# Kernel tuning notes

Hardware: AMD Instinct MI355X
Metric: run time of the kernel (lower is better)

The kernel has to match this reference:

```python
import jax, jax.numpy as jnp
import numpy as np

N_HEADS = 4
N_HIDDEN = 128  # out_features, is_concat=False
NEG_SLOPE = 0.2


def setup_inputs() -> dict:
    key = jax.random.key(0)
    k1, k2, k3, k4 = jax.random.split(key, 4)
    A, S, P, F = 128, 64, 16, 128
    h = jax.random.normal(k1, (A, S, P, F), dtype=jnp.float32)
    # torch Linear(in, out, bias=False): y = x @ W.T ; here we store W already transposed [in, out]
    scale = 1.0 / np.sqrt(F)
    W_l = jax.random.normal(k2, (F, N_HEADS * N_HIDDEN), dtype=jnp.float32) * scale
    W_r = jax.random.normal(k3, (F, N_HEADS * N_HIDDEN), dtype=jnp.float32) * scale
    w_attn = jax.random.normal(k4, (2 * N_HIDDEN,), dtype=jnp.float32) * (1.0 / np.sqrt(2 * N_HIDDEN))
    return {"h": h, "W_l": W_l, "W_r": W_r, "w_attn": w_attn}


def reference(h, W_l, W_r, w_attn):
    A, S, P, F = h.shape
    H, D = N_HEADS, N_HIDDEN
    h_ = jnp.transpose(h, (1, 2, 0, 3))  # [S,P,A,F]
    g_l = (h_ @ W_l).reshape(S, P, A, H, D)
    g_r = (h_ @ W_r).reshape(S, P, A, H, D)
    # attn(cat(g_l[j], g_r[i])) = <w_attn[:D], g_l[j]> + <w_attn[D:], g_r[i]>
    # (single-output Linear over concat, shared across heads) — identical math,
    # avoids materializing the [S,P,A,A,H,2D] concat tensor.
    a_l, a_r = w_attn[:D], w_attn[D:]
    s_l = jnp.einsum('spahd,d->spah', g_l, a_l)  # contributes along j axis
    s_r = jnp.einsum('spahd,d->spah', g_r, a_r)  # contributes along i axis
    e = s_r[:, :, :, None, :] + s_l[:, :, None, :, :]  # [S,P,i,j,H]
    e = jax.nn.leaky_relu(e, negative_slope=NEG_SLOPE)
    diag = jnp.eye(A, dtype=bool)[None, None, :, :, None]  # mask self-edges
    e = jnp.where(diag, -jnp.inf, e)
    a = jax.nn.softmax(e, axis=3)  # softmax over j
    attn_res = jnp.einsum('spijh,spjhd->spihd', a, g_r)  # [S,P,A,H,D]
    attn_res = attn_res.mean(axis=3)  # is_concat=False -> mean over heads
    attn_res = jnp.transpose(attn_res, (2, 0, 1, 3))  # [A,S,P,D]
    return attn_res, a
```

## Files before the change

### kernel.cpp

```cpp
#include <hip/hip_runtime.h>
#include <hip/hip_bf16.h>
#include <stdint.h>


typedef short short8 __attribute__((ext_vector_type(8)));
typedef float f32x4 __attribute__((ext_vector_type(4)));

__device__ __forceinline__ float bf2f(unsigned short u) {
    return __uint_as_float(((unsigned int)u) << 16);
}
__device__ __forceinline__ unsigned short f2bf(float f) {
    unsigned int x = __float_as_uint(f);
    return (unsigned short)((x + 0x7FFFu + ((x >> 16) & 1u)) >> 16);
}
__device__ __forceinline__ float lrelu(float x) {
    return fmaxf(x, 0.2f * x);
}

__global__ void gat_precomp(const float* __restrict__ Wl,
                            const float* __restrict__ Wr,
                            const float* __restrict__ wattn,
                            unsigned short* __restrict__ Wt,
                            float* __restrict__ Vl,
                            float* __restrict__ Vr) {
    int b = blockIdx.x, t = threadIdx.x;
    if (b < 64) {
        int base = b * 1024 + t * 4;
        float4 v = *(const float4*)(Wr + base);
        int f = base >> 9;
        int c = base & 511;
        Wt[(c + 0) * 128 + f] = f2bf(v.x);
        Wt[(c + 1) * 128 + f] = f2bf(v.y);
        Wt[(c + 2) * 128 + f] = f2bf(v.z);
        Wt[(c + 3) * 128 + f] = f2bf(v.w);
    } else {
        const float* W  = (b == 64) ? Wl : Wr;
        const float* aw = wattn + ((b == 64) ? 0 : 128);
        float* V = (b == 64) ? Vl : Vr;
        for (int r = 0; r < 2; ++r) {
            int o = t + r * 256;
            int f = o >> 2, hh = o & 3;
            float acc = 0.f;
            for (int d = 0; d < 128; ++d)
                acc += W[f * 512 + hh * 128 + d] * aw[d];
            V[hh * 128 + f] = acc;
        }
    }
}

__global__ __launch_bounds__(512, 6)
void gat_main(const float* __restrict__ hin,
              const unsigned short* __restrict__ Wt,
              const float* __restrict__ Vl,
              const float* __restrict__ Vr,
              float* __restrict__ out_attn,
              float* __restrict__ out_a) {
    __shared__ __align__(16) unsigned short Gs[128][136];
    __shared__ float sLs[4][132];
    __shared__ float sRs[4][132];
    __shared__ float Ms[4][132];
    __shared__ float Siv[4][132];
    __shared__ float mx1[4], mx2[4];
    __shared__ int   ax1[4];

    const int sp = blockIdx.x;
    const int t = threadIdx.x;
    const int w = t >> 6;
    const int l = t & 63;
    const int q = l >> 4;
    const int ln = l & 15;

    {
        int a = t >> 2, hh = t & 3;
        const float* hr = hin + (size_t)a * 131072 + sp * 128;
        const float* vl = Vl + hh * 128;
        const float* vr = Vr + hh * 128;
        float al = 0.f, ar = 0.f;
        for (int f = 0; f < 128; f += 4) {
            float4 x  = *(const float4*)(hr + f);
            float4 a4 = *(const float4*)(vl + f);
            float4 b4 = *(const float4*)(vr + f);
            al += x.x * a4.x + x.y * a4.y + x.z * a4.z + x.w * a4.w;
            ar += x.x * b4.x + x.y * b4.y + x.z * b4.z + x.w * b4.w;
        }
        sLs[hh][a] = al;
        sRs[hh][a] = ar;
    }
    __syncthreads();

    if (w < 4) {
        float v0 = sLs[w][l], v1 = sLs[w][l + 64];
        float m1, m2; int a1;
        if (v0 >= v1) { m1 = v0; m2 = v1; a1 = l; }
        else          { m1 = v1; m2 = v0; a1 = l + 64; }
        #pragma unroll
        for (int off = 32; off; off >>= 1) {
            float o1 = __shfl_down(m1, off);
            float o2 = __shfl_down(m2, off);
            int   ob = __shfl_down(a1, off);
            if (o1 > m1) { m2 = fmaxf(m1, o2); m1 = o1; a1 = ob; }
            else         { m2 = fmaxf(m2, o1); }
        }
        if (l == 0) { mx1[w] = m1; mx2[w] = m2; ax1[w] = a1; }
    }
    __syncthreads();

    {
        int i = t >> 2, hh = t & 3;
        float sr = sRs[hh][i];
        float Mi = (i == ax1[hh]) ? mx2[hh] : mx1[hh];
        float m = lrelu(sr + Mi);
        float sum = 0.f;
        for (int j = 0; j < 128; ++j) {
            float e = lrelu(sr + sLs[hh][j]);
            sum += __expf(e - m);
        }
        sum -= __expf(lrelu(sr + sLs[hh][i]) - m);
        Ms[hh][i] = m;
        Siv[hh][i] = 1.f / sum;
    }
    __syncthreads();

    {
        float* oa = out_a + (size_t)sp * 65536;
        for (int k = 0; k < 32; ++k) {
            int idx = k * 512 + t;
            int i = idx >> 7, j = idx & 127;
            float4 r4;
            float* rp = (float*)&r4;
            #pragma unroll
            for (int hh = 0; hh < 4; ++hh) {
                float pv = 0.f;
                if (j != i) {
                    float e = lrelu(sRs[hh][i] + sLs[hh][j]);
                    pv = __expf(e - Ms[hh][i]) * Siv[hh][i];
                }
                rp[hh] = pv;
            }
            *(float4*)(oa + (size_t)idx * 4) = r4;
        }
    }

    f32x4 acc[8];
    #pragma unroll
    for (int tj = 0; tj < 8; ++tj) acc[tj] = (f32x4){0.f, 0.f, 0.f, 0.f};

    const float* hrw = hin + (size_t)(16 * w + ln) * 131072 + sp * 128;

    for (int hh = 0; hh < 4; ++hh) {
        __syncthreads();

        short8 axh[4];
        #pragma unroll
        for (int kb = 0; kb < 4; ++kb) {
            float4 xa = *(const float4*)(hrw + 32 * kb + 8 * q);
            float4 xb = *(const float4*)(hrw + 32 * kb + 8 * q + 4);
            short8 v;
            v[0] = (short)f2bf(xa.x); v[1] = (short)f2bf(xa.y);
            v[2] = (short)f2bf(xa.z); v[3] = (short)f2bf(xa.w);
            v[4] = (short)f2bf(xb.x); v[5] = (short)f2bf(xb.y);
            v[6] = (short)f2bf(xb.z); v[7] = (short)f2bf(xb.w);
            axh[kb] = v;
        }

        #pragma unroll
        for (int tj = 0; tj < 8; ++tj) {
            f32x4 g = (f32x4){0.f, 0.f, 0.f, 0.f};
            #pragma unroll
            for (int kb = 0; kb < 4; ++kb) {
                short8 bh = *(const short8*)(Wt + ((hh * 128 + 16 * tj + ln) * 128 + 32 * kb + 8 * q));
                g = __builtin_amdgcn_mfma_f32_16x16x32_bf16(axh[kb], bh, g, 0, 0, 0);
            }
            ushort4 gh4;
            unsigned short* ghp = (unsigned short*)&gh4;
            #pragma unroll
            for (int r = 0; r < 4; ++r) ghp[r] = f2bf(g[r]);
            *(ushort4*)(&Gs[16 * tj + ln][16 * w + 4 * q]) = gh4;
        }
        __syncthreads();

        {
            const int i = 16 * w + ln;
            const float sr = sRs[hh][i];
            const float m = Ms[hh][i];
            const float si = Siv[hh][i];
            #pragma unroll 1
            for (int kb = 0; kb < 4; ++kb) {
                short8 ph, pl;
                #pragma unroll
                for (int jj = 0; jj < 8; ++jj) {
                    int j = 32 * kb + 8 * q + jj;
                    float pv = 0.f;
                    if (j != i) {
                        float e = lrelu(sr + sLs[hh][j]);
                        pv = __expf(e - m) * si;
                    }
                    unsigned short hb = f2bf(pv);
                    ph[jj] = (short)hb;
                    pl[jj] = (short)f2bf(pv - bf2f(hb));
                }
                #pragma unroll
                for (int tj = 0; tj < 8; ++tj) {
                    short8 bh = *(const short8*)(&Gs[16 * tj + ln][32 * kb + 8 * q]);
                    acc[tj] = __builtin_amdgcn_mfma_f32_16x16x32_bf16(ph, bh, acc[tj], 0, 0, 0);
                    acc[tj] = __builtin_amdgcn_mfma_f32_16x16x32_bf16(pl, bh, acc[tj], 0, 0, 0);
                }
            }
        }
    }

    #pragma unroll
    for (int tj = 0; tj < 8; ++tj) {
        int d = 16 * tj + ln;
        #pragma unroll
        for (int r = 0; r < 4; ++r) {
            int i = 16 * w + 4 * q + r;
            out_attn[((size_t)i * 1024 + sp) * 128 + d] = acc[tj][r] * 0.25f;
        }
    }
}

extern "C" void kernel_launch(void* const* d_in, const int* in_sizes, int n_in,
                              void* d_out, int out_size, void* d_ws, size_t ws_size,
                              hipStream_t stream) {
    const float* hin   = (const float*)d_in[0];
    const float* Wl    = (const float*)d_in[1];
    const float* Wr    = (const float*)d_in[2];
    const float* wattn = (const float*)d_in[3];

    unsigned short* Wt = (unsigned short*)d_ws;
    float* Vl = (float*)((char*)d_ws + 131072);
    float* Vr = (float*)((char*)d_ws + 131072 + 2048);

    float* out_attn = (float*)d_out;
    float* out_a    = (float*)d_out + 16777216;

    gat_precomp<<<66, 256, 0, stream>>>(Wl, Wr, wattn, Wt, Vl, Vr);
    gat_main<<<1024, 512, 0, stream>>>(hin, Wt, Vl, Vr, out_attn, out_a);
}
```

Before: 550.1 us.

## Split output feature dimension into halves to cut LDS and registers, raise occupancy

The main aggregation loop now runs twice, once per half of the 128 output features. This halves the shared G tile and the accumulator registers, and the launch bounds are raised from 6 to 8 waves per unit of occupancy. The cost is that the h row loads, bf16 conversion and attention-probability computation are redone for each half, which doubles that work. The precompute dot product and the softmax denominator loop are also vectorised with float4 loads.

```diff
diff --git a/kernel.cpp b/kernel.cpp
--- a/kernel.cpp
+++ b/kernel.cpp
@@ -41,25 +41,29 @@
             int o = t + r * 256;
             int f = o >> 2, hh = o & 3;
             float acc = 0.f;
-            for (int d = 0; d < 128; ++d)
-                acc += W[f * 512 + hh * 128 + d] * aw[d];
+            #pragma unroll 4
+            for (int d = 0; d < 128; d += 4) {
+                float4 wv = *(const float4*)(W + f * 512 + hh * 128 + d);
+                float4 av = *(const float4*)(aw + d);
+                acc += wv.x * av.x + wv.y * av.y + wv.z * av.z + wv.w * av.w;
+            }
             V[hh * 128 + f] = acc;
         }
     }
 }
 
-__global__ __launch_bounds__(512, 6)
+__global__ __launch_bounds__(512, 8)
 void gat_main(const float* __restrict__ hin,
               const unsigned short* __restrict__ Wt,
               const float* __restrict__ Vl,
               const float* __restrict__ Vr,
               float* __restrict__ out_attn,
               float* __restrict__ out_a) {
-    __shared__ __align__(16) unsigned short Gs[128][136];
-    __shared__ float sLs[4][132];
-    __shared__ float sRs[4][132];
-    __shared__ float Ms[4][132];
-    __shared__ float Siv[4][132];
+    __shared__ __align__(16) unsigned short Gs[64][136];
+    __shared__ __align__(16) float sLs[4][132];
+    __shared__ __align__(16) float sRs[4][132];
+    __shared__ __align__(16) float Ms[4][132];
+    __shared__ __align__(16) float Siv[4][132];
     __shared__ float mx1[4], mx2[4];
     __shared__ int   ax1[4];
 
@@ -111,9 +115,12 @@
         float Mi = (i == ax1[hh]) ? mx2[hh] : mx1[hh];
         float m = lrelu(sr + Mi);
         float sum = 0.f;
-        for (int j = 0; j < 128; ++j) {
-            float e = lrelu(sr + sLs[hh][j]);
-            sum += __expf(e - m);
+        for (int j4 = 0; j4 < 128; j4 += 4) {
+            float4 sl4 = *(const float4*)(&sLs[hh][j4]);
+            sum += __expf(lrelu(sr + sl4.x) - m);
+            sum += __expf(lrelu(sr + sl4.y) - m);
+            sum += __expf(lrelu(sr + sl4.z) - m);
+            sum += __expf(lrelu(sr + sl4.w) - m);
         }
         sum -= __expf(lrelu(sr + sLs[hh][i]) - m);
         Ms[hh][i] = m;
@@ -141,81 +148,83 @@
         }
     }
 
-    f32x4 acc[8];
-    #pragma unroll
-    for (int tj = 0; tj < 8; ++tj) acc[tj] = (f32x4){0.f, 0.f, 0.f, 0.f};
-
     const float* hrw = hin + (size_t)(16 * w + ln) * 131072 + sp * 128;
-
-    for (int hh = 0; hh < 4; ++hh) {
-        __syncthreads();
-
-        short8 axh[4];
+    const int irow = 16 * w + ln;
+
+    for (int half = 0; half < 2; ++half) {
+        f32x4 acc4[4];
         #pragma unroll
-        for (int kb = 0; kb < 4; ++kb) {
-            float4 xa = *(const float4*)(hrw + 32 * kb + 8 * q);
-            float4 xb = *(const float4*)(hrw + 32 * kb + 8 * q + 4);
-            short8 v;
-            v[0] = (short)f2bf(xa.x); v[1] = (short)f2bf(xa.y);
-            v[2] = (short)f2bf(xa.z); v[3] = (short)f2bf(xa.w);
-            v[4] = (short)f2bf(xb.x); v[5] = (short)f2bf(xb.y);
-            v[6] = (short)f2bf(xb.z); v[7] = (short)f2bf(xb.w);
-            axh[kb] = v;
+        for (int tjh = 0; tjh < 4; ++tjh) acc4[tjh] = (f32x4){0.f, 0.f, 0.f, 0.f};
+
+        for (int hh = 0; hh < 4; ++hh) {
+            __syncthreads();
+
+            short8 axh[4];
+            #pragma unroll
+            for (int kb = 0; kb < 4; ++kb) {
+                float4 xa = *(const float4*)(hrw + 32 * kb + 8 * q);
+                float4 xb = *(const float4*)(hrw + 32 * kb + 8 * q + 4);
+                short8 v;
+                v[0] = (short)f2bf(xa.x); v[1] = (short)f2bf(xa.y);
+                v[2] = (short)f2bf(xa.z); v[3] = (short)f2bf(xa.w);
+                v[4] = (short)f2bf(xb.x); v[5] = (short)f2bf(xb.y);
+                v[6] = (short)f2bf(xb.z); v[7] = (short)f2bf(xb.w);
+                axh[kb] = v;
+            }
+
+            #pragma unroll
+            for (int tjh = 0; tjh < 4; ++tjh) {
+                f32x4 g = (f32x4){0.f, 0.f, 0.f, 0.f};
+                #pragma unroll
+                for (int kb = 0; kb < 4; ++kb) {
+                    short8 bh = *(const short8*)(Wt + ((hh * 128 + 64 * half + 16 * tjh + ln) * 128 + 32 * kb + 8 * q));
+                    g = __builtin_amdgcn_mfma_f32_16x16x32_bf16(axh[kb], bh, g, 0, 0, 0);
+                }
+                ushort4 gh4;
+                unsigned short* ghp = (unsigned short*)&gh4;
+                #pragma unroll
+                for (int r = 0; r < 4; ++r) ghp[r] = f2bf(g[r]);
+                *(ushort4*)(&Gs[16 * tjh + ln][16 * w + 4 * q]) = gh4;
+            }
+            __syncthreads();
+
+            {
+                const float sr = sRs[hh][irow];
+                const float m = Ms[hh][irow];
+                const float si = Siv[hh][irow];
+                #pragma unroll 1
+                for (int kb = 0; kb < 4; ++kb) {
+                    short8 ph, pl;
+                    #pragma unroll
+                    for (int jj = 0; jj < 8; ++jj) {
+                        int j = 32 * kb + 8 * q + jj;
+                        float pv = 0.f;
+                        if (j != irow) {
+                            float e = lrelu(sr + sLs[hh][j]);
+                            pv = __expf(e - m) * si;
+                        }
+                        unsigned short hb = f2bf(pv);
+                        ph[jj] = (short)hb;
+                        pl[jj] = (short)f2bf(pv - bf2f(hb));
+                    }
+                    #pragma unroll
+                    for (int tjh = 0; tjh < 4; ++tjh) {
+                        short8 bh = *(const short8*)(&Gs[16 * tjh + ln][32 * kb + 8 * q]);
+                        acc4[tjh] = __builtin_amdgcn_mfma_f32_16x16x32_bf16(ph, bh, acc4[tjh], 0, 0, 0);
+                        acc4[tjh] = __builtin_amdgcn_mfma_f32_16x16x32_bf16(pl, bh, acc4[tjh], 0, 0, 0);
+                    }
+                }
+            }
         }
 
         #pragma unroll
-        for (int tj = 0; tj < 8; ++tj) {
-            f32x4 g = (f32x4){0.f, 0.f, 0.f, 0.f};
-            #pragma unroll
-            for (int kb = 0; kb < 4; ++kb) {
-                short8 bh = *(const short8*)(Wt + ((hh * 128 + 16 * tj + ln) * 128 + 32 * kb + 8 * q));
-                g = __builtin_amdgcn_mfma_f32_16x16x32_bf16(axh[kb], bh, g, 0, 0, 0);
-            }
-            ushort4 gh4;
-            unsigned short* ghp = (unsigned short*)&gh4;
-            #pragma unroll
-            for (int r = 0; r < 4; ++r) ghp[r] = f2bf(g[r]);
-            *(ushort4*)(&Gs[16 * tj + ln][16 * w + 4 * q]) = gh4;
-        }
-        __syncthreads();
-
-        {
-            const int i = 16 * w + ln;
-            const float sr = sRs[hh][i];
-            const float m = Ms[hh][i];
-            const float si = Siv[hh][i];
-            #pragma unroll 1
-            for (int kb = 0; kb < 4; ++kb) {
-                short8 ph, pl;
-                #pragma unroll
-                for (int jj = 0; jj < 8; ++jj) {
-                    int j = 32 * kb + 8 * q + jj;
-                    float pv = 0.f;
-                    if (j != i) {
-                        float e = lrelu(sr + sLs[hh][j]);
-                        pv = __expf(e - m) * si;
-                    }
-                    unsigned short hb = f2bf(pv);
-                    ph[jj] = (short)hb;
-                    pl[jj] = (short)f2bf(pv - bf2f(hb));
-                }
-                #pragma unroll
-                for (int tj = 0; tj < 8; ++tj) {
-                    short8 bh = *(const short8*)(&Gs[16 * tj + ln][32 * kb + 8 * q]);
-                    acc[tj] = __builtin_amdgcn_mfma_f32_16x16x32_bf16(ph, bh, acc[tj], 0, 0, 0);
-                    acc[tj] = __builtin_amdgcn_mfma_f32_16x16x32_bf16(pl, bh, acc[tj], 0, 0, 0);
-                }
-            }
-        }
-    }
-
-    #pragma unroll
-    for (int tj = 0; tj < 8; ++tj) {
-        int d = 16 * tj + ln;
-        #pragma unroll
-        for (int r = 0; r < 4; ++r) {
-            int i = 16 * w + 4 * q + r;
-            out_attn[((size_t)i * 1024 + sp) * 128 + d] = acc[tj][r] * 0.25f;
+        for (int tjh = 0; tjh < 4; ++tjh) {
+            int d = 64 * half + 16 * tjh + ln;
+            #pragma unroll
+            for (int r = 0; r < 4; ++r) {
+                int i = 16 * w + 4 * q + r;
+                out_attn[((size_t)i * 1024 + sp) * 128 + d] = acc4[tjh][r] * 0.25f;
+            }
         }
     }
 }
```

New measurement: 556.1 us. No clear change (+1.1%).
